# Performance work log

Measured on AMD Instinct MI355X. Metric: run time of the kernel, lower is better.

The kernel has to match this reference:

```python
import jax, jax.numpy as jnp
import numpy as np
import math

B, T, D = 48, 4096, 256
K_TIMES = 1
# replicate torch module's stage/block computation (static Python math)
_ns = (int(math.log(T)) + 1) * K_TIMES          # 9
BLOCK = int(T / _ns)                             # 455
if T % _ns != 0:
    N_STAGES = int(T / BLOCK) + 1                # 10
    PAD = N_STAGES * BLOCK - T                   # 454
else:
    N_STAGES, PAD = _ns, 0


def setup_inputs() -> dict:
    key = jax.random.key(0)
    k1, k2 = jax.random.split(key)
    x = jax.random.normal(k1, (B, T, D), dtype=jnp.float32)
    # fusion linear: in=2D, out=D (torch Linear weight [out,in])
    W_fuse = jax.random.normal(k2, (D, 2 * D), dtype=jnp.float32) * (1.0 / np.sqrt(2 * D))
    b_fuse = jnp.zeros((D,), dtype=jnp.float32)
    return {"x": x, "W_fuse": W_fuse, "b_fuse": b_fuse}


def _attention(q, k, v):
    # q: [..., Lq, D], k/v: [..., Lk, D]
    scores = jnp.matmul(q, jnp.swapaxes(k, -2, -1)) / jnp.sqrt(jnp.asarray(q.shape[-1], q.dtype))
    p = jax.nn.softmax(scores, axis=-1)
    return jnp.matmul(p, v)


def reference(x, W_fuse, b_fuse):
    xp = jnp.pad(x, ((0, 0), (0, PAD), (0, 0)))                      # [B, N_STAGES*BLOCK, D]
    chunked = xp.reshape(B * N_STAGES, BLOCK, D)                      # [B*S, BLOCK, D]
    q = jnp.max(chunked, axis=1).reshape(B, N_STAGES, D)              # block summaries [B, S, D]
    q_block = _attention(q, q, q)                                     # [B, S, D]
    q_step = _attention(q_block.reshape(B * N_STAGES, 1, D), chunked, chunked)
    q_step = q_step.reshape(B, N_STAGES, D)                           # [B, S, D]
    fused = jnp.concatenate([q_block, q_step], axis=-1)               # [B, S, 2D]
    return jnp.einsum('bsf,df->bsd', fused, W_fuse) + b_fuse
```

## Files before the change

kernel.cpp:

```cpp
#include <hip/hip_runtime.h>
#include <math.h>

#define NB 48
#define NT 4096
#define ND 256
#define NS 10
#define BLK 455

__global__ __launch_bounds__(256) void kmax(const float* __restrict__ x,
                                            float* __restrict__ q) {
    const int bs = blockIdx.x;
    const int b = bs / NS, s = bs % NS;
    const int g  = threadIdx.x & 63;
    const int rs = threadIdx.x >> 6;
    const long base = ((long)b * NT + (long)s * BLK) * ND;
    const int nrows = min(BLK, NT - s * BLK);

    float4 m;
    if (nrows < BLK) m = make_float4(0.f, 0.f, 0.f, 0.f);
    else             m = make_float4(-INFINITY, -INFINITY, -INFINITY, -INFINITY);

    for (int r = rs; r < nrows; r += 4) {
        const float4 v = *reinterpret_cast<const float4*>(x + base + (long)r * ND + g * 4);
        m.x = fmaxf(m.x, v.x); m.y = fmaxf(m.y, v.y);
        m.z = fmaxf(m.z, v.z); m.w = fmaxf(m.w, v.w);
    }

    __shared__ float4 red[4][64];
    red[rs][g] = m;
    __syncthreads();
    if (rs == 0) {
        float4 a = red[0][g];
        #pragma unroll
        for (int k = 1; k < 4; ++k) {
            float4 o = red[k][g];
            a.x = fmaxf(a.x, o.x); a.y = fmaxf(a.y, o.y);
            a.z = fmaxf(a.z, o.z); a.w = fmaxf(a.w, o.w);
        }
        *reinterpret_cast<float4*>(q + (long)bs * ND + g * 4) = a;
    }
}

__global__ __launch_bounds__(256) void kqblock(const float* __restrict__ q,
                                               float* __restrict__ qb) {
    const int b = blockIdx.x;
    const int tid = threadIdx.x;
    __shared__ float sq[NS][ND];
    __shared__ float sp[NS][NS];

    for (int i = tid; i < NS * ND; i += 256)
        sq[i / ND][i % ND] = q[(long)b * NS * ND + i];
    __syncthreads();

    if (tid < NS * NS) {
        const int i = tid / NS, j = tid % NS;
        float acc = 0.f;
        for (int d = 0; d < ND; ++d) acc += sq[i][d] * sq[j][d];
        sp[i][j] = acc * 0.0625f;
    }
    __syncthreads();

    if (tid < NS) {
        float m = -INFINITY;
        for (int j = 0; j < NS; ++j) m = fmaxf(m, sp[tid][j]);
        float sum = 0.f;
        for (int j = 0; j < NS; ++j) { float e = expf(sp[tid][j] - m); sp[tid][j] = e; sum += e; }
        const float inv = 1.f / sum;
        for (int j = 0; j < NS; ++j) sp[tid][j] *= inv;
    }
    __syncthreads();

    for (int i = 0; i < NS; ++i) {
        float acc = 0.f;
        #pragma unroll
        for (int j = 0; j < NS; ++j) acc += sp[i][j] * sq[j][tid];
        qb[((long)b * NS + i) * ND + tid] = acc;
    }
}

__global__ __launch_bounds__(256) void kstep(const float* __restrict__ x,
                                             const float* __restrict__ qb,
                                             float* __restrict__ qs) {
    const int bs = blockIdx.x;
    const int b = bs / NS, s = bs % NS;
    const int tid  = threadIdx.x;
    const int lane = tid & 63;
    const int w    = tid >> 6;
    const long base = ((long)b * NT + (long)s * BLK) * ND;
    const int nrows = min(BLK, NT - s * BLK);
    const int npad  = BLK - nrows;

    const float4 qb4 = *reinterpret_cast<const float4*>(qb + (long)bs * ND + lane * 4);

    __shared__ float sc[BLK];
    __shared__ float rbuf[256];

    for (int r = w; r < nrows; r += 4) {
        const float4 v = *reinterpret_cast<const float4*>(x + base + (long)r * ND + lane * 4);
        float p = v.x * qb4.x + v.y * qb4.y + v.z * qb4.z + v.w * qb4.w;
        #pragma unroll
        for (int o = 32; o; o >>= 1) p += __shfl_xor(p, o);
        if (lane == 0) sc[r] = p * 0.0625f;
    }
    __syncthreads();

    float m = (npad > 0) ? 0.f : -INFINITY;
    for (int r = tid; r < nrows; r += 256) m = fmaxf(m, sc[r]);
    rbuf[tid] = m;
    __syncthreads();
    for (int o = 128; o; o >>= 1) {
        if (tid < o) rbuf[tid] = fmaxf(rbuf[tid], rbuf[tid + o]);
        __syncthreads();
    }
    m = rbuf[0];
    __syncthreads();

    float sum = 0.f;
    for (int r = tid; r < nrows; r += 256) {
        const float e = expf(sc[r] - m);
        sc[r] = e;
        sum += e;
    }
    rbuf[tid] = sum;
    __syncthreads();
    for (int o = 128; o; o >>= 1) {
        if (tid < o) rbuf[tid] += rbuf[tid + o];
        __syncthreads();
    }
    const float denom = rbuf[0] + (float)npad * expf(-m);

    float4 acc = make_float4(0.f, 0.f, 0.f, 0.f);
    for (int r = w; r < nrows; r += 4) {
        const float4 v = *reinterpret_cast<const float4*>(x + base + (long)r * ND + lane * 4);
        const float p = sc[r];
        acc.x += p * v.x; acc.y += p * v.y;
        acc.z += p * v.z; acc.w += p * v.w;
    }
    __shared__ float4 r4[4][64];
    r4[w][lane] = acc;
    __syncthreads();
    if (w == 0) {
        float4 a = r4[0][lane];
        #pragma unroll
        for (int k = 1; k < 4; ++k) {
            float4 o = r4[k][lane];
            a.x += o.x; a.y += o.y; a.z += o.z; a.w += o.w;
        }
        const float inv = 1.f / denom;
        a.x *= inv; a.y *= inv; a.z *= inv; a.w *= inv;
        *reinterpret_cast<float4*>(qs + (long)bs * ND + lane * 4) = a;
    }
}

__global__ __launch_bounds__(256) void kout(const float* __restrict__ qb,
                                            const float* __restrict__ qs,
                                            const float* __restrict__ Wf,
                                            const float* __restrict__ bf,
                                            float* __restrict__ out) {
    const int bs = blockIdx.x;
    const int tid = threadIdx.x;
    __shared__ float f[2 * ND];
    f[tid]      = qb[(long)bs * ND + tid];
    f[ND + tid] = qs[(long)bs * ND + tid];
    __syncthreads();

    const float* wr = Wf + (long)tid * 2 * ND;
    float acc = bf[tid];
    for (int k = 0; k < 2 * ND; k += 4) {
        const float4 w4 = *reinterpret_cast<const float4*>(wr + k);
        acc += f[k] * w4.x + f[k + 1] * w4.y + f[k + 2] * w4.z + f[k + 3] * w4.w;
    }
    out[(long)bs * ND + tid] = acc;
}

extern "C" void kernel_launch(void* const* d_in, const int* in_sizes, int n_in,
                              void* d_out, int out_size, void* d_ws, size_t ws_size,
                              hipStream_t stream) {
    const float* x  = (const float*)d_in[0];
    const float* Wf = (const float*)d_in[1];
    const float* bf = (const float*)d_in[2];
    float* out = (float*)d_out;

    float* q  = (float*)d_ws;
    float* qb = q  + NB * NS * ND;
    float* qs = qb + NB * NS * ND;

    kmax  <<<NB * NS, 256, 0, stream>>>(x, q);
    kqblock<<<NB,      256, 0, stream>>>(q, qb);
    kstep <<<NB * NS, 256, 0, stream>>>(x, qb, qs);
    kout  <<<NB * NS, 256, 0, stream>>>(qb, qs, Wf, bf, out);
}
```

Baseline: 422.6 us.

## Split block reductions into four partial blocks with online-softmax merge

The max-pool and step-attention kernels now split each 455-row block across four workgroups, raising the grid from 480 to 1920 workgroups to fill more CUs. The step kernel uses a single-pass online softmax, so x is read once instead of twice, and writes partial (max, sum, acc) triples. A final kernel merges the partials and applies the fusion linear. The cost is extra workspace traffic for partials plus per-row exp rescaling in the online loop.

```diff
diff --git a/kernel.cpp b/kernel.cpp
--- a/kernel.cpp
+++ b/kernel.cpp
@@ -6,50 +6,62 @@
 #define ND 256
 #define NS 10
 #define BLK 455
-
-__global__ __launch_bounds__(256) void kmax(const float* __restrict__ x,
-                                            float* __restrict__ q) {
-    const int bs = blockIdx.x;
+#define NP 4
+#define RPP 114
+
+__global__ __launch_bounds__(256) void kmaxp(const float* __restrict__ x,
+                                             float* __restrict__ qpart) {
+    const int bsp = blockIdx.x;
+    const int p  = bsp & 3;
+    const int bs = bsp >> 2;
     const int b = bs / NS, s = bs % NS;
-    const int g  = threadIdx.x & 63;
-    const int rs = threadIdx.x >> 6;
-    const long base = ((long)b * NT + (long)s * BLK) * ND;
+    const int start = p * RPP;
+    const int len   = min(BLK - start, RPP);
     const int nrows = min(BLK, NT - s * BLK);
-
-    float4 m;
-    if (nrows < BLK) m = make_float4(0.f, 0.f, 0.f, 0.f);
-    else             m = make_float4(-INFINITY, -INFINITY, -INFINITY, -INFINITY);
-
-    for (int r = rs; r < nrows; r += 4) {
+    const int nreal = max(0, min(nrows - start, len));
+    const int npad  = len - nreal;
+    const int g = threadIdx.x & 63;
+    const int w = threadIdx.x >> 6;
+    const long base = ((long)b * NT + (long)s * BLK + start) * ND;
+
+    float4 m = (npad > 0) ? make_float4(0.f, 0.f, 0.f, 0.f)
+                          : make_float4(-INFINITY, -INFINITY, -INFINITY, -INFINITY);
+    for (int r = w; r < nreal; r += 4) {
         const float4 v = *reinterpret_cast<const float4*>(x + base + (long)r * ND + g * 4);
         m.x = fmaxf(m.x, v.x); m.y = fmaxf(m.y, v.y);
         m.z = fmaxf(m.z, v.z); m.w = fmaxf(m.w, v.w);
     }
 
     __shared__ float4 red[4][64];
-    red[rs][g] = m;
-    __syncthreads();
-    if (rs == 0) {
+    red[w][g] = m;
+    __syncthreads();
+    if (w == 0) {
         float4 a = red[0][g];
         #pragma unroll
         for (int k = 1; k < 4; ++k) {
-            float4 o = red[k][g];
+            const float4 o = red[k][g];
             a.x = fmaxf(a.x, o.x); a.y = fmaxf(a.y, o.y);
             a.z = fmaxf(a.z, o.z); a.w = fmaxf(a.w, o.w);
         }
-        *reinterpret_cast<float4*>(q + (long)bs * ND + g * 4) = a;
-    }
-}
-
-__global__ __launch_bounds__(256) void kqblock(const float* __restrict__ q,
+        *reinterpret_cast<float4*>(qpart + (long)bsp * ND + g * 4) = a;
+    }
+}
+
+__global__ __launch_bounds__(256) void kqblock(const float* __restrict__ qpart,
                                                float* __restrict__ qb) {
     const int b = blockIdx.x;
     const int tid = threadIdx.x;
     __shared__ float sq[NS][ND];
     __shared__ float sp[NS][NS];
 
-    for (int i = tid; i < NS * ND; i += 256)
-        sq[i / ND][i % ND] = q[(long)b * NS * ND + i];
+    for (int i = tid; i < NS * ND; i += 256) {
+        const int st = i / ND, d = i % ND;
+        const long base = ((long)(b * NS + st) * NP) * ND + d;
+        float v = qpart[base];
+        #pragma unroll
+        for (int p = 1; p < NP; ++p) v = fmaxf(v, qpart[base + (long)p * ND]);
+        sq[st][d] = v;
+    }
     __syncthreads();
 
     if (tid < NS * NS) {
@@ -64,7 +76,7 @@
         float m = -INFINITY;
         for (int j = 0; j < NS; ++j) m = fmaxf(m, sp[tid][j]);
         float sum = 0.f;
-        for (int j = 0; j < NS; ++j) { float e = expf(sp[tid][j] - m); sp[tid][j] = e; sum += e; }
+        for (int j = 0; j < NS; ++j) { const float e = expf(sp[tid][j] - m); sp[tid][j] = e; sum += e; }
         const float inv = 1.f / sum;
         for (int j = 0; j < NS; ++j) sp[tid][j] *= inv;
     }
@@ -78,99 +90,106 @@
     }
 }
 
-__global__ __launch_bounds__(256) void kstep(const float* __restrict__ x,
-                                             const float* __restrict__ qb,
-                                             float* __restrict__ qs) {
+__global__ __launch_bounds__(256) void kstepp(const float* __restrict__ x,
+                                              const float* __restrict__ qb,
+                                              float* __restrict__ mpart,
+                                              float* __restrict__ lpart,
+                                              float* __restrict__ accpart) {
+    const int bsp = blockIdx.x;
+    const int p  = bsp & 3;
+    const int bs = bsp >> 2;
+    const int b = bs / NS, s = bs % NS;
+    const int start = p * RPP;
+    const int len   = min(BLK - start, RPP);
+    const int nrows = min(BLK, NT - s * BLK);
+    const int nreal = max(0, min(nrows - start, len));
+    const int npad  = len - nreal;
+    const int lane = threadIdx.x & 63;
+    const int w    = threadIdx.x >> 6;
+    const long base = ((long)b * NT + (long)s * BLK + start) * ND;
+
+    const float4 qb4 = *reinterpret_cast<const float4*>(qb + (long)bs * ND + lane * 4);
+
+    float m = -INFINITY, l = 0.f;
+    float4 acc = make_float4(0.f, 0.f, 0.f, 0.f);
+
+    for (int r = w; r < nreal; r += 4) {
+        const float4 v = *reinterpret_cast<const float4*>(x + base + (long)r * ND + lane * 4);
+        float sc = v.x * qb4.x + v.y * qb4.y + v.z * qb4.z + v.w * qb4.w;
+        #pragma unroll
+        for (int o = 32; o; o >>= 1) sc += __shfl_xor(sc, o);
+        sc *= 0.0625f;
+        if (sc > m) {
+            const float g = expf(m - sc);
+            l *= g; acc.x *= g; acc.y *= g; acc.z *= g; acc.w *= g;
+            m = sc;
+        }
+        const float e = expf(sc - m);
+        l += e;
+        acc.x += e * v.x; acc.y += e * v.y;
+        acc.z += e * v.z; acc.w += e * v.w;
+    }
+
+    __shared__ float  sm[4], sl[4];
+    __shared__ float4 sacc[4][64];
+    if (lane == 0) { sm[w] = m; sl[w] = l; }
+    sacc[w][lane] = acc;
+    __syncthreads();
+
+    if (w == 0) {
+        float mp = (npad > 0) ? 0.f : -INFINITY;
+        #pragma unroll
+        for (int k = 0; k < 4; ++k) mp = fmaxf(mp, sm[k]);
+        float lf = (float)npad * expf(-mp);
+        float4 af = make_float4(0.f, 0.f, 0.f, 0.f);
+        #pragma unroll
+        for (int k = 0; k < 4; ++k) {
+            const float g = expf(sm[k] - mp);
+            lf += sl[k] * g;
+            const float4 o = sacc[k][lane];
+            af.x += o.x * g; af.y += o.y * g;
+            af.z += o.z * g; af.w += o.w * g;
+        }
+        if (lane == 0) { mpart[bsp] = mp; lpart[bsp] = lf; }
+        *reinterpret_cast<float4*>(accpart + (long)bsp * ND + lane * 4) = af;
+    }
+}
+
+__global__ __launch_bounds__(256) void kfinal(const float* __restrict__ qb,
+                                              const float* __restrict__ mpart,
+                                              const float* __restrict__ lpart,
+                                              const float* __restrict__ accpart,
+                                              const float* __restrict__ Wf,
+                                              const float* __restrict__ bf,
+                                              float* __restrict__ out) {
     const int bs = blockIdx.x;
-    const int b = bs / NS, s = bs % NS;
-    const int tid  = threadIdx.x;
-    const int lane = tid & 63;
-    const int w    = tid >> 6;
-    const long base = ((long)b * NT + (long)s * BLK) * ND;
-    const int nrows = min(BLK, NT - s * BLK);
-    const int npad  = BLK - nrows;
-
-    const float4 qb4 = *reinterpret_cast<const float4*>(qb + (long)bs * ND + lane * 4);
-
-    __shared__ float sc[BLK];
-    __shared__ float rbuf[256];
-
-    for (int r = w; r < nrows; r += 4) {
-        const float4 v = *reinterpret_cast<const float4*>(x + base + (long)r * ND + lane * 4);
-        float p = v.x * qb4.x + v.y * qb4.y + v.z * qb4.z + v.w * qb4.w;
-        #pragma unroll
-        for (int o = 32; o; o >>= 1) p += __shfl_xor(p, o);
-        if (lane == 0) sc[r] = p * 0.0625f;
-    }
-    __syncthreads();
-
-    float m = (npad > 0) ? 0.f : -INFINITY;
-    for (int r = tid; r < nrows; r += 256) m = fmaxf(m, sc[r]);
-    rbuf[tid] = m;
-    __syncthreads();
-    for (int o = 128; o; o >>= 1) {
-        if (tid < o) rbuf[tid] = fmaxf(rbuf[tid], rbuf[tid + o]);
-        __syncthreads();
-    }
-    m = rbuf[0];
-    __syncthreads();
-
-    float sum = 0.f;
-    for (int r = tid; r < nrows; r += 256) {
-        const float e = expf(sc[r] - m);
-        sc[r] = e;
-        sum += e;
-    }
-    rbuf[tid] = sum;
-    __syncthreads();
-    for (int o = 128; o; o >>= 1) {
-        if (tid < o) rbuf[tid] += rbuf[tid + o];
-        __syncthreads();
-    }
-    const float denom = rbuf[0] + (float)npad * expf(-m);
-
-    float4 acc = make_float4(0.f, 0.f, 0.f, 0.f);
-    for (int r = w; r < nrows; r += 4) {
-        const float4 v = *reinterpret_cast<const float4*>(x + base + (long)r * ND + lane * 4);
-        const float p = sc[r];
-        acc.x += p * v.x; acc.y += p * v.y;
-        acc.z += p * v.z; acc.w += p * v.w;
-    }
-    __shared__ float4 r4[4][64];
-    r4[w][lane] = acc;
-    __syncthreads();
-    if (w == 0) {
-        float4 a = r4[0][lane];
-        #pragma unroll
-        for (int k = 1; k < 4; ++k) {
-            float4 o = r4[k][lane];
-            a.x += o.x; a.y += o.y; a.z += o.z; a.w += o.w;
-        }
-        const float inv = 1.f / denom;
-        a.x *= inv; a.y *= inv; a.z *= inv; a.w *= inv;
-        *reinterpret_cast<float4*>(qs + (long)bs * ND + lane * 4) = a;
-    }
-}
-
-__global__ __launch_bounds__(256) void kout(const float* __restrict__ qb,
-                                            const float* __restrict__ qs,
-                                            const float* __restrict__ Wf,
-                                            const float* __restrict__ bf,
-                                            float* __restrict__ out) {
-    const int bs = blockIdx.x;
-    const int tid = threadIdx.x;
+    const int d = threadIdx.x;
+
+    const float m0 = mpart[bs * NP + 0], m1 = mpart[bs * NP + 1];
+    const float m2 = mpart[bs * NP + 2], m3 = mpart[bs * NP + 3];
+    const float mm = fmaxf(fmaxf(m0, m1), fmaxf(m2, m3));
+    const float s0 = expf(m0 - mm), s1 = expf(m1 - mm);
+    const float s2 = expf(m2 - mm), s3 = expf(m3 - mm);
+    const float l = lpart[bs * NP + 0] * s0 + lpart[bs * NP + 1] * s1
+                  + lpart[bs * NP + 2] * s2 + lpart[bs * NP + 3] * s3;
+    const float a = accpart[((long)bs * NP + 0) * ND + d] * s0
+                  + accpart[((long)bs * NP + 1) * ND + d] * s1
+                  + accpart[((long)bs * NP + 2) * ND + d] * s2
+                  + accpart[((long)bs * NP + 3) * ND + d] * s3;
+    const float qs = a / l;
+
     __shared__ float f[2 * ND];
-    f[tid]      = qb[(long)bs * ND + tid];
-    f[ND + tid] = qs[(long)bs * ND + tid];
-    __syncthreads();
-
-    const float* wr = Wf + (long)tid * 2 * ND;
-    float acc = bf[tid];
+    f[d]      = qb[(long)bs * ND + d];
+    f[ND + d] = qs;
+    __syncthreads();
+
+    const float* wr = Wf + (long)d * 2 * ND;
+    float acc = bf[d];
     for (int k = 0; k < 2 * ND; k += 4) {
         const float4 w4 = *reinterpret_cast<const float4*>(wr + k);
         acc += f[k] * w4.x + f[k + 1] * w4.y + f[k + 2] * w4.z + f[k + 3] * w4.w;
     }
-    out[(long)bs * ND + tid] = acc;
+    out[(long)bs * ND + d] = acc;
 }
 
 extern "C" void kernel_launch(void* const* d_in, const int* in_sizes, int n_in,
@@ -181,12 +200,14 @@
     const float* bf = (const float*)d_in[2];
     float* out = (float*)d_out;
 
-    float* q  = (float*)d_ws;
-    float* qb = q  + NB * NS * ND;
-    float* qs = qb + NB * NS * ND;
-
-    kmax  <<<NB * NS, 256, 0, stream>>>(x, q);
-    kqblock<<<NB,      256, 0, stream>>>(q, qb);
-    kstep <<<NB * NS, 256, 0, stream>>>(x, qb, qs);
-    kout  <<<NB * NS, 256, 0, stream>>>(qb, qs, Wf, bf, out);
-}
+    float* qpart   = (float*)d_ws;
+    float* accpart = qpart + NB * NS * NP * ND;
+    float* qb      = accpart + NB * NS * NP * ND;
+    float* mpart   = qb + NB * NS * ND;
+    float* lpart   = mpart + NB * NS * NP;
+
+    kmaxp  <<<NB * NS * NP, 256, 0, stream>>>(x, qpart);
+    kqblock<<<NB,           256, 0, stream>>>(qpart, qb);
+    kstepp <<<NB * NS * NP, 256, 0, stream>>>(x, qb, mpart, lpart, accpart);
+    kfinal <<<NB * NS,      256, 0, stream>>>(qb, mpart, lpart, accpart, Wf, bf, out);
+}
```

New measurement: 350.6 us. 17.0% less time.
